# Kernel optimization log

Measured on AMD Instinct MI355X. Metric: run time of the kernel, lower is better.

Reference implementation:

```python
import jax, jax.numpy as jnp
import numpy as np

EPSILON = 0.1
MAX_ITER = 50

def setup_inputs() -> dict:
    key = jax.random.key(0)
    kx, ky = jax.random.split(key)
    x = jax.random.normal(kx, (16, 1024, 256), dtype=jnp.float32)
    y = jax.random.normal(ky, (16, 1024, 256), dtype=jnp.float32)
    return {"x": x, "y": y}

def _cdist(x, y):
    # pairwise euclidean distance, (B, Lx, Ly)
    x2 = jnp.sum(x * x, axis=-1)  # (B, Lx)
    y2 = jnp.sum(y * y, axis=-1)  # (B, Ly)
    xy = jnp.einsum('bld,bmd->blm', x, y)
    d2 = x2[:, :, None] + y2[:, None, :] - 2.0 * xy
    return jnp.sqrt(jnp.maximum(d2, 0.0))

def reference(x, y):
    cost = _cdist(x, y)                      # (B, Lx, Ly)
    B, Lx, Ly = cost.shape
    log_mu = jnp.full((B, Lx), -jnp.log(jnp.float32(Lx)), dtype=cost.dtype)
    log_nu = jnp.full((B, Ly), -jnp.log(jnp.float32(Ly)), dtype=cost.dtype)
    log_k = -cost / EPSILON                  # (B, Lx, Ly)

    def body(carry, _):
        log_u, log_v = carry
        log_u = log_mu - jax.scipy.special.logsumexp(log_k + log_v[:, None, :], axis=2)
        log_v = log_nu - jax.scipy.special.logsumexp(log_k + log_u[:, :, None], axis=1)
        return (log_u, log_v), None

    init = (jnp.zeros((B, Lx), cost.dtype), jnp.zeros((B, Ly), cost.dtype))
    (log_u, log_v), _ = jax.lax.scan(body, init, None, length=MAX_ITER)

    # transport = u * exp(log_k) * v, fused in log space
    transport = jnp.exp(log_u[:, :, None] + log_k + log_v[:, None, :])
    distance = jnp.sum(transport * cost, axis=(1, 2))  # (B,)
    return jnp.mean(distance)
```

## Files before the change

### kernel.cpp

```cpp
#include <hip/hip_runtime.h>
#include <math.h>

#define NB 16
#define L 1024
#define D 256
#define N_ITER 50
#define LOG_MU (-6.9314718055994531f)
#define QSCALE 2560.0f
#define QS (1.0f/256.0f)
#define QSC (1.0f/2560.0f)

typedef short short4_t __attribute__((ext_vector_type(4)));

__global__ __launch_bounds__(256) void norms_kernel(
    const float* __restrict__ x, const float* __restrict__ y,
    float* __restrict__ x2, float* __restrict__ y2) {
  int wid = threadIdx.x >> 6, lane = threadIdx.x & 63;
  int row = blockIdx.x * 4 + wid;
  const float* src = (row < NB * L) ? (x + (size_t)row * D)
                                    : (y + (size_t)(row - NB * L) * D);
  float4 v = *(const float4*)(src + lane * 4);
  float s = v.x * v.x + v.y * v.y + v.z * v.z + v.w * v.w;
  #pragma unroll
  for (int off = 32; off; off >>= 1) s += __shfl_down(s, off);
  if (lane == 0) {
    if (row < NB * L) x2[row] = s;
    else              y2[row - NB * L] = s;
  }
}

__global__ __launch_bounds__(256) void anchor_kernel(
    const float* __restrict__ x, const float* __restrict__ y,
    const float* __restrict__ x2, const float* __restrict__ y2,
    float* __restrict__ anchor) {
  int w = threadIdx.x >> 6, lane = threadIdx.x & 63;
  int gr = blockIdx.x * 4 + w;
  int b = gr >> 10, i = gr & 1023;
  const float* xr = x + (size_t)gr * D;
  float4 xv = *(const float4*)(xr + lane * 4);
  float dots[16];
  #pragma unroll
  for (int s = 0; s < 16; ++s) {
    int j = (i + s * 64 + s * s) & 1023;
    float4 yv = *(const float4*)(y + ((size_t)b * L + j) * D + lane * 4);
    dots[s] = xv.x * yv.x + xv.y * yv.y + xv.z * yv.z + xv.w * yv.w;
  }
  #pragma unroll
  for (int s = 0; s < 16; ++s)
    #pragma unroll
    for (int off = 32; off; off >>= 1) dots[s] += __shfl_xor(dots[s], off);
  if (lane == 0) {
    float xx = x2[gr];
    float mn = 3.4e38f;
    #pragma unroll
    for (int s = 0; s < 16; ++s) {
      int j = (i + s * 64 + s * s) & 1023;
      float d2 = xx + y2[b * L + j] - 2.0f * dots[s];
      mn = fminf(mn, sqrtf(fmaxf(d2, 0.0f)));
    }
    anchor[gr] = mn;
  }
}

__global__ __launch_bounds__(256) void costq_kernel(
    const float* __restrict__ x, const float* __restrict__ y,
    const float* __restrict__ x2, const float* __restrict__ y2,
    const float* __restrict__ anchor, short* __restrict__ Q) {
  __shared__ float xs[16][68];
  __shared__ float ys[16][68];
  int bid = blockIdx.x;
  int b = bid >> 8;
  int rem = bid & 255;
  int i0 = (rem >> 4) << 6;
  int j0 = (rem & 15) << 6;
  int tid = threadIdx.x;
  int tx = tid & 15, ty = tid >> 4;
  int r = tid >> 2, kq = tid & 3;

  float acc[4][4] = {};
  const float* xbase = x + ((size_t)b * L + i0 + r) * D + kq * 4;
  const float* ybase = y + ((size_t)b * L + j0 + r) * D + kq * 4;
  for (int k0 = 0; k0 < D; k0 += 16) {
    float4 xv = *(const float4*)(xbase + k0);
    float4 yv = *(const float4*)(ybase + k0);
    __syncthreads();
    xs[kq * 4 + 0][r] = xv.x; xs[kq * 4 + 1][r] = xv.y;
    xs[kq * 4 + 2][r] = xv.z; xs[kq * 4 + 3][r] = xv.w;
    ys[kq * 4 + 0][r] = yv.x; ys[kq * 4 + 1][r] = yv.y;
    ys[kq * 4 + 2][r] = yv.z; ys[kq * 4 + 3][r] = yv.w;
    __syncthreads();
    #pragma unroll
    for (int kk = 0; kk < 16; ++kk) {
      float4 av = *(const float4*)&xs[kk][ty * 4];
      float4 bv = *(const float4*)&ys[kk][tx * 4];
      float a[4] = {av.x, av.y, av.z, av.w};
      float bb[4] = {bv.x, bv.y, bv.z, bv.w};
      #pragma unroll
      for (int er = 0; er < 4; ++er)
        #pragma unroll
        for (int ec = 0; ec < 4; ++ec)
          acc[er][ec] = fmaf(a[er], bb[ec], acc[er][ec]);
    }
  }
  float xr[4], yc[4], ar[4];
  #pragma unroll
  for (int e = 0; e < 4; ++e) {
    xr[e] = x2[b * L + i0 + ty * 4 + e];
    yc[e] = y2[b * L + j0 + tx * 4 + e];
    ar[e] = anchor[b * L + i0 + ty * 4 + e];
  }
  #pragma unroll
  for (int er = 0; er < 4; ++er) {
    short4_t q4;
    #pragma unroll
    for (int ec = 0; ec < 4; ++ec) {
      float d2 = xr[er] + yc[ec] - 2.0f * acc[er][ec];
      float c = sqrtf(fmaxf(d2, 0.0f));
      int qi = __float2int_rn((ar[er] - c) * QSCALE);
      q4[ec] = (short)min(max(qi, -32767), 32767);
    }
    *(short4_t*)(Q + ((size_t)b * L + i0 + ty * 4 + er) * L + j0 + tx * 4) = q4;
  }
}

__global__ __launch_bounds__(256) void pass_fused_kernel(
    const short* __restrict__ Q, const float* __restrict__ anchor,
    const float* __restrict__ vin, float* __restrict__ uout,
    float* __restrict__ partial) {
  __shared__ float4 cacc[4][256];
  int bb = blockIdx.x;
  int w = threadIdx.x >> 6, lane = threadIdx.x & 63;
  int b = bb >> 6;
  const float4* g4 = (const float4*)(vin + (b << 10));
  float vv[16];
  float4 a0 = g4[lane * 2], a1 = g4[lane * 2 + 1];
  float4 a2 = g4[128 + lane * 2], a3 = g4[128 + lane * 2 + 1];
  vv[0]=a0.x; vv[1]=a0.y; vv[2]=a0.z; vv[3]=a0.w;
  vv[4]=a1.x; vv[5]=a1.y; vv[6]=a1.z; vv[7]=a1.w;
  vv[8]=a2.x; vv[9]=a2.y; vv[10]=a2.z; vv[11]=a2.w;
  vv[12]=a3.x; vv[13]=a3.y; vv[14]=a3.z; vv[15]=a3.w;
  float m = vv[0];
  #pragma unroll
  for (int t = 1; t < 16; ++t) m = fmaxf(m, vv[t]);
  #pragma unroll
  for (int off = 32; off; off >>= 1) m = fmaxf(m, __shfl_xor(m, off));
  #pragma unroll
  for (int t = 0; t < 16; ++t) vv[t] -= m;
  float E = __expf(LOG_MU - m);
  float colacc[16] = {};

  #define T8(base, V4)                                                   \
    t[base+0] = __expf(fmaf((float)(short)(V4.x), QS, vv[base+0]));      \
    t[base+1] = __expf(fmaf((float)((V4.x) >> 16), QS, vv[base+1]));     \
    t[base+2] = __expf(fmaf((float)(short)(V4.y), QS, vv[base+2]));      \
    t[base+3] = __expf(fmaf((float)((V4.y) >> 16), QS, vv[base+3]));     \
    t[base+4] = __expf(fmaf((float)(short)(V4.z), QS, vv[base+4]));      \
    t[base+5] = __expf(fmaf((float)(V4.z) >> 16), QS, vv[base+5]));      \
    t[base+6] = __expf(fmaf((float)(short)(V4.w), QS, vv[base+6]));      \
    t[base+7] = __expf(fmaf((float)((V4.w) >> 16), QS, vv[base+7]));

  #pragma unroll
  for (int rr = 0; rr < 4; ++rr) {
    int r = bb * 16 + rr * 4 + w;
    const int4* q0 = (const int4*)(Q + (size_t)r * L);
    int4 cA = q0[lane], cB = q0[64 + lane];
    float t[16];
    t[0]  = __expf(fmaf((float)(short)(cA.x), QS, vv[0]));
    t[1]  = __expf(fmaf((float)(cA.x >> 16),  QS, vv[1]));
    t[2]  = __expf(fmaf((float)(short)(cA.y), QS, vv[2]));
    t[3]  = __expf(fmaf((float)(cA.y >> 16),  QS, vv[3]));
    t[4]  = __expf(fmaf((float)(short)(cA.z), QS, vv[4]));
    t[5]  = __expf(fmaf((float)(cA.z >> 16),  QS, vv[5]));
    t[6]  = __expf(fmaf((float)(short)(cA.w), QS, vv[6]));
    t[7]  = __expf(fmaf((float)(cA.w >> 16),  QS, vv[7]));
    t[8]  = __expf(fmaf((float)(short)(cB.x), QS, vv[8]));
    t[9]  = __expf(fmaf((float)(cB.x >> 16),  QS, vv[9]));
    t[10] = __expf(fmaf((float)(short)(cB.y), QS, vv[10]));
    t[11] = __expf(fmaf((float)(cB.y >> 16),  QS, vv[11]));
    t[12] = __expf(fmaf((float)(short)(cB.z), QS, vv[12]));
    t[13] = __expf(fmaf((float)(cB.z >> 16),  QS, vv[13]));
    t[14] = __expf(fmaf((float)(short)(cB.w), QS, vv[14]));
    t[15] = __expf(fmaf((float)(cB.w >> 16),  QS, vv[15]));
    float racc = 0.0f;
    #pragma unroll
    for (int k = 0; k < 16; ++k) racc += t[k];
    #pragma unroll
    for (int off = 32; off; off >>= 1) racc += __shfl_xor(racc, off);
    if (lane == 0)
      uout[r] = LOG_MU + fmaf(10.0f, anchor[r], -m) - __logf(racc);
    float g = E / racc;
    #pragma unroll
    for (int k = 0; k < 16; ++k) colacc[k] = fmaf(t[k], g, colacc[k]);
  }
  cacc[w][lane * 2]       = {colacc[0], colacc[1], colacc[2], colacc[3]};
  cacc[w][lane * 2 + 1]   = {colacc[4], colacc[5], colacc[6], colacc[7]};
  cacc[w][128 + lane * 2]     = {colacc[8], colacc[9], colacc[10], colacc[11]};
  cacc[w][128 + lane * 2 + 1] = {colacc[12], colacc[13], colacc[14], colacc[15]};
  __syncthreads();
  int tid = threadIdx.x;
  float4 s0 = cacc[0][tid], s1 = cacc[1][tid], s2 = cacc[2][tid], s3 = cacc[3][tid];
  float4 s = {s0.x + s1.x + s2.x + s3.x, s0.y + s1.y + s2.y + s3.y,
              s0.z + s1.z + s2.z + s3.z, s0.w + s1.w + s2.w + s3.w};
  ((float4*)partial)[bb * 256 + tid] = s;
}

__global__ __launch_bounds__(256) void reducev_kernel(
    const float* __restrict__ partial, const float* __restrict__ vin,
    float* __restrict__ vout) {
  __shared__ float red[4];
  int b = blockIdx.x >> 2;
  int tid = threadIdx.x;
  const float* vb = vin + (b << 10);
  float m = fmaxf(fmaxf(vb[tid], vb[tid + 256]), fmaxf(vb[tid + 512], vb[tid + 768]));
  #pragma unroll
  for (int off = 32; off; off >>= 1) m = fmaxf(m, __shfl_xor(m, off));
  int w = tid >> 6;
  if ((tid & 63) == 0) red[w] = m;
  __syncthreads();
  m = fmaxf(fmaxf(red[0], red[1]), fmaxf(red[2], red[3]));
  int j = ((blockIdx.x & 3) << 8) + tid;
  const float* p = partial + (((size_t)b << 6) << 10) + j;
  float s = 0.0f;
  #pragma unroll
  for (int k = 0; k < 64; ++k) s += p[k << 10];
  vout[(b << 10) + j] = LOG_MU - __logf(s) + vb[j] - m;
}

__global__ __launch_bounds__(256) void distance_kernel(
    const short* __restrict__ Q, const float* __restrict__ anchor,
    const float* __restrict__ lu, const float* __restrict__ lv,
    float* __restrict__ pdist) {
  __shared__ float red[4];
  int bb = blockIdx.x;
  int w = threadIdx.x >> 6, lane = threadIdx.x & 63;
  int b = bb >> 6;
  const float4* g4 = (const float4*)(lv + (b << 10));
  float vv[16];
  float4 a0 = g4[lane * 2], a1 = g4[lane * 2 + 1];
  float4 a2 = g4[128 + lane * 2], a3 = g4[128 + lane * 2 + 1];
  vv[0]=a0.x; vv[1]=a0.y; vv[2]=a0.z; vv[3]=a0.w;
  vv[4]=a1.x; vv[5]=a1.y; vv[6]=a1.z; vv[7]=a1.w;
  vv[8]=a2.x; vv[9]=a2.y; vv[10]=a2.z; vv[11]=a2.w;
  vv[12]=a3.x; vv[13]=a3.y; vv[14]=a3.z; vv[15]=a3.w;
  float m = vv[0];
  #pragma unroll
  for (int t = 1; t < 16; ++t) m = fmaxf(m, vv[t]);
  #pragma unroll
  for (int off = 32; off; off >>= 1) m = fmaxf(m, __shfl_xor(m, off));
  #pragma unroll
  for (int t = 0; t < 16; ++t) vv[t] -= m;

  float racc = 0.0f;
  #pragma unroll
  for (int rr = 0; rr < 4; ++rr) {
    int r = bb * 16 + rr * 4 + w;
    float ar = anchor[r];
    float A = fmaf(-10.0f, ar, lu[r]) + m;
    float va[16];
    #pragma unroll
    for (int k = 0; k < 16; ++k) va[k] = vv[k] + A;
    const int4* q0 = (const int4*)(Q + (size_t)r * L);
    int4 cA = q0[lane], cB = q0[64 + lane];
    #define DACC(V, B)                                                      \
      { float qf = (float)(short)(V);                                       \
        float e = __expf(fmaf(qf, QS, va[B]));                              \
        racc = fmaf(e, fmaf(qf, -QSC, ar), racc);                           \
        qf = (float)((V) >> 16);                                            \
        e = __expf(fmaf(qf, QS, va[(B) + 1]));                              \
        racc = fmaf(e, fmaf(qf, -QSC, ar), racc); }
    DACC(cA.x, 0) DACC(cA.y, 2) DACC(cA.z, 4) DACC(cA.w, 6)
    DACC(cB.x, 8) DACC(cB.y, 10) DACC(cB.z, 12) DACC(cB.w, 14)
    #undef DACC
  }
  #pragma unroll
  for (int off = 32; off; off >>= 1) racc += __shfl_xor(racc, off);
  if (lane == 0) red[w] = racc;
  __syncthreads();
  if (threadIdx.x == 0) pdist[bb] = red[0] + red[1] + red[2] + red[3];
}

__global__ __launch_bounds__(256) void finalred_kernel(
    const float* __restrict__ pdist, float* __restrict__ out) {
  __shared__ float red[4];
  int tid = threadIdx.x;
  float s = pdist[tid] + pdist[tid + 256] + pdist[tid + 512] + pdist[tid + 768];
  #pragma unroll
  for (int off = 32; off; off >>= 1) s += __shfl_xor(s, off);
  int w = tid >> 6;
  if ((tid & 63) == 0) red[w] = s;
  __syncthreads();
  if (tid == 0) out[0] = (red[0] + red[1] + red[2] + red[3]) * (1.0f / NB);
}

extern "C" void kernel_launch(void* const* d_in, const int* in_sizes, int n_in,
                              void* d_out, int out_size, void* d_ws, size_t ws_size,
                              hipStream_t stream) {
  const float* x = (const float*)d_in[0];
  const float* y = (const float*)d_in[1];
  float* out = (float*)d_out;
  char* ws = (char*)d_ws;

  const size_t szQ = (size_t)NB * L * L * sizeof(short);
  const size_t szP = (size_t)NB * 64 * L * sizeof(float);
  short* Q = (short*)ws;
  float* partial = (float*)(ws + szQ);
  float* x2 = (float*)(ws + szQ + szP);
  float* y2 = x2 + NB * L;
  float* anchor = y2 + NB * L;
  float* lu = anchor + NB * L;
  float* lv = lu + NB * L;
  float* pdist = lv + NB * L;

  hipMemsetAsync(lv, 0, NB * L * sizeof(float), stream);

  norms_kernel<<<2 * NB * L / 4, 256, 0, stream>>>(x, y, x2, y2);
  anchor_kernel<<<NB * L / 4, 256, 0, stream>>>(x, y, x2, y2, anchor);
  costq_kernel<<<NB * 256, 256, 0, stream>>>(x, y, x2, y2, anchor, Q);

  for (int t = 0; t < N_ITER; ++t) {
    pass_fused_kernel<<<NB * L / 16, 256, 0, stream>>>(Q, anchor, lv, lu, partial);
    reducev_kernel<<<NB * L / 256, 256, 0, stream>>>(partial, lv, lv);
  }
  distance_kernel<<<NB * L / 16, 256, 0, stream>>>(Q, anchor, lu, lv, pdist);
  finalred_kernel<<<1, 256, 0, stream>>>(pdist, out);
}
```

Before: 835.0 us.

## Switch to base-2 log domain, fp16 cost storage, precomputed block maxima

Stores the quantized cost as fp16 instead of int16 and runs the Sinkhorn potentials in base-2 log space, so exp2f replaces __expf with the scale folded into constants. The per-batch max of v is now produced by reducev as 16 block maxima instead of a full 1024-wide max reduction in every pass block. reducev is split into more blocks with shared-memory partial sums, Q row loads are all issued up front, and costq gets register prefetch of the next k-slice. The fp16 encoding changes quantization precision relative to the int16 scheme.

```diff
diff --git a/kernel.cpp b/kernel.cpp
--- a/kernel.cpp
+++ b/kernel.cpp
@@ -1,14 +1,17 @@
 #include <hip/hip_runtime.h>
+#include <hip/hip_fp16.h>
 #include <math.h>
 
 #define NB 16
 #define L 1024
 #define D 256
 #define N_ITER 50
-#define LOG_MU (-6.9314718055994531f)
 #define QSCALE 2560.0f
-#define QS (1.0f/256.0f)
 #define QSC (1.0f/2560.0f)
+#define LOG2E 1.4426950408889634f
+#define QS2 (LOG2E/256.0f)
+#define LOG_MU2 (-10.0f)
+#define TEN_LOG2E 14.426950408889634f
 
 typedef short short4_t __attribute__((ext_vector_type(4)));
 
@@ -32,7 +35,7 @@
 __global__ __launch_bounds__(256) void anchor_kernel(
     const float* __restrict__ x, const float* __restrict__ y,
     const float* __restrict__ x2, const float* __restrict__ y2,
-    float* __restrict__ anchor) {
+    float* __restrict__ anchor, float* __restrict__ A2) {
   int w = threadIdx.x >> 6, lane = threadIdx.x & 63;
   int gr = blockIdx.x * 4 + w;
   int b = gr >> 10, i = gr & 1023;
@@ -59,13 +62,14 @@
       mn = fminf(mn, sqrtf(fmaxf(d2, 0.0f)));
     }
     anchor[gr] = mn;
+    A2[gr] = mn * TEN_LOG2E;
   }
 }
 
 __global__ __launch_bounds__(256) void costq_kernel(
     const float* __restrict__ x, const float* __restrict__ y,
     const float* __restrict__ x2, const float* __restrict__ y2,
-    const float* __restrict__ anchor, short* __restrict__ Q) {
+    const float* __restrict__ anchor, __half* __restrict__ Q) {
   __shared__ float xs[16][68];
   __shared__ float ys[16][68];
   int bid = blockIdx.x;
@@ -80,9 +84,12 @@
   float acc[4][4] = {};
   const float* xbase = x + ((size_t)b * L + i0 + r) * D + kq * 4;
   const float* ybase = y + ((size_t)b * L + j0 + r) * D + kq * 4;
+  float4 xv = *(const float4*)(xbase);
+  float4 yv = *(const float4*)(ybase);
   for (int k0 = 0; k0 < D; k0 += 16) {
-    float4 xv = *(const float4*)(xbase + k0);
-    float4 yv = *(const float4*)(ybase + k0);
+    int kn = (k0 + 16) & 255;
+    float4 nx = *(const float4*)(xbase + kn);
+    float4 ny = *(const float4*)(ybase + kn);
     __syncthreads();
     xs[kq * 4 + 0][r] = xv.x; xs[kq * 4 + 1][r] = xv.y;
     xs[kq * 4 + 2][r] = xv.z; xs[kq * 4 + 3][r] = xv.w;
@@ -101,6 +108,7 @@
         for (int ec = 0; ec < 4; ++ec)
           acc[er][ec] = fmaf(a[er], bb[ec], acc[er][ec]);
     }
+    xv = nx; yv = ny;
   }
   float xr[4], yc[4], ar[4];
   #pragma unroll
@@ -116,167 +124,201 @@
     for (int ec = 0; ec < 4; ++ec) {
       float d2 = xr[er] + yc[ec] - 2.0f * acc[er][ec];
       float c = sqrtf(fmaxf(d2, 0.0f));
-      int qi = __float2int_rn((ar[er] - c) * QSCALE);
-      q4[ec] = (short)min(max(qi, -32767), 32767);
+      float qv = fminf(fmaxf((ar[er] - c) * QSCALE, -30000.0f), 30000.0f);
+      __half h = __float2half(qv);
+      q4[ec] = __half_as_short(h);
     }
-    *(short4_t*)(Q + ((size_t)b * L + i0 + ty * 4 + er) * L + j0 + tx * 4) = q4;
-  }
-}
+    *(short4_t*)((short*)Q + ((size_t)b * L + i0 + ty * 4 + er) * L + j0 + tx * 4) = q4;
+  }
+}
+
+#define DEC2(word, base)                                           \
+  { __half2 h2 = *reinterpret_cast<const __half2*>(&(word));       \
+    float2 f2 = __half22float2(h2);                                \
+    t[base]     = exp2f(fmaf(f2.x, QS2, vv[base]));                \
+    t[base + 1] = exp2f(fmaf(f2.y, QS2, vv[base + 1])); }
 
 __global__ __launch_bounds__(256) void pass_fused_kernel(
-    const short* __restrict__ Q, const float* __restrict__ anchor,
-    const float* __restrict__ vin, float* __restrict__ uout,
-    float* __restrict__ partial) {
+    const __half* __restrict__ Q, const float* __restrict__ A2,
+    const float* __restrict__ v2, const float* __restrict__ bmax,
+    float* __restrict__ u2out, float* __restrict__ partial) {
   __shared__ float4 cacc[4][256];
   int bb = blockIdx.x;
-  int w = threadIdx.x >> 6, lane = threadIdx.x & 63;
+  int tid = threadIdx.x;
+  int w = tid >> 6, lane = tid & 63;
   int b = bb >> 6;
-  const float4* g4 = (const float4*)(vin + (b << 10));
-  float vv[16];
+  int r0 = bb * 16 + w;
+
+  const int4* q0 = (const int4*)(Q + (size_t)r0 * L);
+  const int4* q1 = (const int4*)(Q + (size_t)(r0 + 4) * L);
+  const int4* q2 = (const int4*)(Q + (size_t)(r0 + 8) * L);
+  const int4* q3 = (const int4*)(Q + (size_t)(r0 + 12) * L);
+  int4 cA0 = q0[lane], cB0 = q0[64 + lane];
+  int4 cA1 = q1[lane], cB1 = q1[64 + lane];
+  int4 cA2 = q2[lane], cB2 = q2[64 + lane];
+  int4 cA3 = q3[lane], cB3 = q3[64 + lane];
+
+  const float* bm = bmax + b * 16;
+  float m2 = bm[0];
+  #pragma unroll
+  for (int k = 1; k < 16; ++k) m2 = fmaxf(m2, bm[k]);
+
+  const float4* g4 = (const float4*)(v2 + (b << 10));
   float4 a0 = g4[lane * 2], a1 = g4[lane * 2 + 1];
   float4 a2 = g4[128 + lane * 2], a3 = g4[128 + lane * 2 + 1];
+  float vv[16];
+  vv[0]=a0.x-m2; vv[1]=a0.y-m2; vv[2]=a0.z-m2; vv[3]=a0.w-m2;
+  vv[4]=a1.x-m2; vv[5]=a1.y-m2; vv[6]=a1.z-m2; vv[7]=a1.w-m2;
+  vv[8]=a2.x-m2; vv[9]=a2.y-m2; vv[10]=a2.z-m2; vv[11]=a2.w-m2;
+  vv[12]=a3.x-m2; vv[13]=a3.y-m2; vv[14]=a3.z-m2; vv[15]=a3.w-m2;
+  float E2 = exp2f(LOG_MU2 - m2);
+  float colacc[16] = {};
+  float r_0, r_1, r_2, r_3;
+
+#define ROWP(cA_, cB_, ROUT)                                              \
+  { float t[16];                                                          \
+    DEC2(cA_.x, 0) DEC2(cA_.y, 2) DEC2(cA_.z, 4) DEC2(cA_.w, 6)           \
+    DEC2(cB_.x, 8) DEC2(cB_.y, 10) DEC2(cB_.z, 12) DEC2(cB_.w, 14)        \
+    float racc = ((t[0]+t[1])+(t[2]+t[3])) + ((t[4]+t[5])+(t[6]+t[7]))    \
+               + ((t[8]+t[9])+(t[10]+t[11])) + ((t[12]+t[13])+(t[14]+t[15])); \
+    _Pragma("unroll")                                                     \
+    for (int off = 32; off; off >>= 1) racc += __shfl_xor(racc, off);     \
+    float g = E2 / racc;                                                  \
+    _Pragma("unroll")                                                     \
+    for (int k = 0; k < 16; ++k) colacc[k] = fmaf(t[k], g, colacc[k]);    \
+    ROUT = racc; }
+
+  ROWP(cA0, cB0, r_0)
+  ROWP(cA1, cB1, r_1)
+  ROWP(cA2, cB2, r_2)
+  ROWP(cA3, cB3, r_3)
+#undef ROWP
+
+  if (lane == 0) {
+    u2out[r0]      = LOG_MU2 + A2[r0]      - m2 - log2f(r_0);
+    u2out[r0 + 4]  = LOG_MU2 + A2[r0 + 4]  - m2 - log2f(r_1);
+    u2out[r0 + 8]  = LOG_MU2 + A2[r0 + 8]  - m2 - log2f(r_2);
+    u2out[r0 + 12] = LOG_MU2 + A2[r0 + 12] - m2 - log2f(r_3);
+  }
+  cacc[w][lane * 2]           = {colacc[0], colacc[1], colacc[2], colacc[3]};
+  cacc[w][lane * 2 + 1]       = {colacc[4], colacc[5], colacc[6], colacc[7]};
+  cacc[w][128 + lane * 2]     = {colacc[8], colacc[9], colacc[10], colacc[11]};
+  cacc[w][128 + lane * 2 + 1] = {colacc[12], colacc[13], colacc[14], colacc[15]};
+  __syncthreads();
+  float4 s0 = cacc[0][tid], s1 = cacc[1][tid], s2 = cacc[2][tid], s3 = cacc[3][tid];
+  float4 s = {s0.x + s1.x + s2.x + s3.x, s0.y + s1.y + s2.y + s3.y,
+              s0.z + s1.z + s2.z + s3.z, s0.w + s1.w + s2.w + s3.w};
+  ((float4*)partial)[bb * 256 + tid] = s;
+}
+
+__global__ __launch_bounds__(256) void reducev_kernel(
+    const float* __restrict__ partial, float* __restrict__ v2,
+    const float* __restrict__ bmax_cur, float* __restrict__ bmax_next) {
+  __shared__ float ss[4][64];
+  int blk = blockIdx.x;
+  int b = blk >> 4;
+  int j0 = (blk & 15) << 6;
+  int tid = threadIdx.x;
+  int c = tid & 63, q = tid >> 6;
+  const float* p = partial + (((size_t)b * 64 + q * 16) << 10) + j0 + c;
+  float s = 0.0f;
+  #pragma unroll
+  for (int k = 0; k < 16; ++k) s += p[(size_t)k << 10];
+  ss[q][c] = s;
+  __syncthreads();
+  if (tid < 64) {
+    const float* bm = bmax_cur + b * 16;
+    float m2 = bm[0];
+    #pragma unroll
+    for (int k = 1; k < 16; ++k) m2 = fmaxf(m2, bm[k]);
+    float S = ss[0][c] + ss[1][c] + ss[2][c] + ss[3][c];
+    int j = (b << 10) + j0 + c;
+    float vn = LOG_MU2 - log2f(S) + v2[j] - m2;
+    v2[j] = vn;
+    float mx = vn;
+    #pragma unroll
+    for (int off = 32; off; off >>= 1) mx = fmaxf(mx, __shfl_xor(mx, off));
+    if (c == 0) bmax_next[blk] = mx;
+  }
+}
+
+__global__ __launch_bounds__(256) void distance_kernel(
+    const __half* __restrict__ Q, const float* __restrict__ anchor,
+    const float* __restrict__ A2, const float* __restrict__ u2,
+    const float* __restrict__ v2, float* __restrict__ pdist) {
+  __shared__ float red[4];
+  int bb = blockIdx.x;
+  int tid = threadIdx.x;
+  int w = tid >> 6, lane = tid & 63;
+  int b = bb >> 6;
+  int r0 = bb * 16 + w;
+  const int4* q0 = (const int4*)(Q + (size_t)r0 * L);
+  const int4* q1 = (const int4*)(Q + (size_t)(r0 + 4) * L);
+  const int4* q2 = (const int4*)(Q + (size_t)(r0 + 8) * L);
+  const int4* q3 = (const int4*)(Q + (size_t)(r0 + 12) * L);
+  int4 cA0 = q0[lane], cB0 = q0[64 + lane];
+  int4 cA1 = q1[lane], cB1 = q1[64 + lane];
+  int4 cA2 = q2[lane], cB2 = q2[64 + lane];
+  int4 cA3 = q3[lane], cB3 = q3[64 + lane];
+
+  const float4* g4 = (const float4*)(v2 + (b << 10));
+  float4 a0 = g4[lane * 2], a1 = g4[lane * 2 + 1];
+  float4 a2 = g4[128 + lane * 2], a3 = g4[128 + lane * 2 + 1];
+  float vv[16];
   vv[0]=a0.x; vv[1]=a0.y; vv[2]=a0.z; vv[3]=a0.w;
   vv[4]=a1.x; vv[5]=a1.y; vv[6]=a1.z; vv[7]=a1.w;
   vv[8]=a2.x; vv[9]=a2.y; vv[10]=a2.z; vv[11]=a2.w;
   vv[12]=a3.x; vv[13]=a3.y; vv[14]=a3.z; vv[15]=a3.w;
-  float m = vv[0];
-  #pragma unroll
-  for (int t = 1; t < 16; ++t) m = fmaxf(m, vv[t]);
-  #pragma unroll
-  for (int off = 32; off; off >>= 1) m = fmaxf(m, __shfl_xor(m, off));
-  #pragma unroll
-  for (int t = 0; t < 16; ++t) vv[t] -= m;
-  float E = __expf(LOG_MU - m);
-  float colacc[16] = {};
-
-  #define T8(base, V4)                                                   \
-    t[base+0] = __expf(fmaf((float)(short)(V4.x), QS, vv[base+0]));      \
-    t[base+1] = __expf(fmaf((float)((V4.x) >> 16), QS, vv[base+1]));     \
-    t[base+2] = __expf(fmaf((float)(short)(V4.y), QS, vv[base+2]));      \
-    t[base+3] = __expf(fmaf((float)((V4.y) >> 16), QS, vv[base+3]));     \
-    t[base+4] = __expf(fmaf((float)(short)(V4.z), QS, vv[base+4]));      \
-    t[base+5] = __expf(fmaf((float)(V4.z) >> 16), QS, vv[base+5]));      \
-    t[base+6] = __expf(fmaf((float)(short)(V4.w), QS, vv[base+6]));      \
-    t[base+7] = __expf(fmaf((float)((V4.w) >> 16), QS, vv[base+7]));
-
-  #pragma unroll
-  for (int rr = 0; rr < 4; ++rr) {
-    int r = bb * 16 + rr * 4 + w;
-    const int4* q0 = (const int4*)(Q + (size_t)r * L);
-    int4 cA = q0[lane], cB = q0[64 + lane];
-    float t[16];
-    t[0]  = __expf(fmaf((float)(short)(cA.x), QS, vv[0]));
-    t[1]  = __expf(fmaf((float)(cA.x >> 16),  QS, vv[1]));
-    t[2]  = __expf(fmaf((float)(short)(cA.y), QS, vv[2]));
-    t[3]  = __expf(fmaf((float)(cA.y >> 16),  QS, vv[3]));
-    t[4]  = __expf(fmaf((float)(short)(cA.z), QS, vv[4]));
-    t[5]  = __expf(fmaf((float)(cA.z >> 16),  QS, vv[5]));
-    t[6]  = __expf(fmaf((float)(short)(cA.w), QS, vv[6]));
-    t[7]  = __expf(fmaf((float)(cA.w >> 16),  QS, vv[7]));
-    t[8]  = __expf(fmaf((float)(short)(cB.x), QS, vv[8]));
-    t[9]  = __expf(fmaf((float)(cB.x >> 16),  QS, vv[9]));
-    t[10] = __expf(fmaf((float)(short)(cB.y), QS, vv[10]));
-    t[11] = __expf(fmaf((float)(cB.y >> 16),  QS, vv[11]));
-    t[12] = __expf(fmaf((float)(short)(cB.z), QS, vv[12]));
-    t[13] = __expf(fmaf((float)(cB.z >> 16),  QS, vv[13]));
-    t[14] = __expf(fmaf((float)(short)(cB.w), QS, vv[14]));
-    t[15] = __expf(fmaf((float)(cB.w >> 16),  QS, vv[15]));
-    float racc = 0.0f;
-    #pragma unroll
-    for (int k = 0; k < 16; ++k) racc += t[k];
-    #pragma unroll
-    for (int off = 32; off; off >>= 1) racc += __shfl_xor(racc, off);
-    if (lane == 0)
-      uout[r] = LOG_MU + fmaf(10.0f, anchor[r], -m) - __logf(racc);
-    float g = E / racc;
-    #pragma unroll
-    for (int k = 0; k < 16; ++k) colacc[k] = fmaf(t[k], g, colacc[k]);
-  }
-  cacc[w][lane * 2]       = {colacc[0], colacc[1], colacc[2], colacc[3]};
-  cacc[w][lane * 2 + 1]   = {colacc[4], colacc[5], colacc[6], colacc[7]};
-  cacc[w][128 + lane * 2]     = {colacc[8], colacc[9], colacc[10], colacc[11]};
-  cacc[w][128 + lane * 2 + 1] = {colacc[12], colacc[13], colacc[14], colacc[15]};
-  __syncthreads();
-  int tid = threadIdx.x;
-  float4 s0 = cacc[0][tid], s1 = cacc[1][tid], s2 = cacc[2][tid], s3 = cacc[3][tid];
-  float4 s = {s0.x + s1.x + s2.x + s3.x, s0.y + s1.y + s2.y + s3.y,
-              s0.z + s1.z + s2.z + s3.z, s0.w + s1.w + s2.w + s3.w};
-  ((float4*)partial)[bb * 256 + tid] = s;
-}
-
-__global__ __launch_bounds__(256) void reducev_kernel(
-    const float* __restrict__ partial, const float* __restrict__ vin,
-    float* __restrict__ vout) {
-  __shared__ float red[4];
-  int b = blockIdx.x >> 2;
-  int tid = threadIdx.x;
-  const float* vb = vin + (b << 10);
-  float m = fmaxf(fmaxf(vb[tid], vb[tid + 256]), fmaxf(vb[tid + 512], vb[tid + 768]));
-  #pragma unroll
-  for (int off = 32; off; off >>= 1) m = fmaxf(m, __shfl_xor(m, off));
-  int w = tid >> 6;
-  if ((tid & 63) == 0) red[w] = m;
-  __syncthreads();
-  m = fmaxf(fmaxf(red[0], red[1]), fmaxf(red[2], red[3]));
-  int j = ((blockIdx.x & 3) << 8) + tid;
-  const float* p = partial + (((size_t)b << 6) << 10) + j;
-  float s = 0.0f;
-  #pragma unroll
-  for (int k = 0; k < 64; ++k) s += p[k << 10];
-  vout[(b << 10) + j] = LOG_MU - __logf(s) + vb[j] - m;
-}
-
-__global__ __launch_bounds__(256) void distance_kernel(
-    const short* __restrict__ Q, const float* __restrict__ anchor,
-    const float* __restrict__ lu, const float* __restrict__ lv,
-    float* __restrict__ pdist) {
-  __shared__ float red[4];
-  int bb = blockIdx.x;
-  int w = threadIdx.x >> 6, lane = threadIdx.x & 63;
-  int b = bb >> 6;
-  const float4* g4 = (const float4*)(lv + (b << 10));
-  float vv[16];
-  float4 a0 = g4[lane * 2], a1 = g4[lane * 2 + 1];
-  float4 a2 = g4[128 + lane * 2], a3 = g4[128 + lane * 2 + 1];
-  vv[0]=a0.x; vv[1]=a0.y; vv[2]=a0.z; vv[3]=a0.w;
-  vv[4]=a1.x; vv[5]=a1.y; vv[6]=a1.z; vv[7]=a1.w;
-  vv[8]=a2.x; vv[9]=a2.y; vv[10]=a2.z; vv[11]=a2.w;
-  vv[12]=a3.x; vv[13]=a3.y; vv[14]=a3.z; vv[15]=a3.w;
-  float m = vv[0];
-  #pragma unroll
-  for (int t = 1; t < 16; ++t) m = fmaxf(m, vv[t]);
-  #pragma unroll
-  for (int off = 32; off; off >>= 1) m = fmaxf(m, __shfl_xor(m, off));
-  #pragma unroll
-  for (int t = 0; t < 16; ++t) vv[t] -= m;
 
   float racc = 0.0f;
-  #pragma unroll
-  for (int rr = 0; rr < 4; ++rr) {
-    int r = bb * 16 + rr * 4 + w;
-    float ar = anchor[r];
-    float A = fmaf(-10.0f, ar, lu[r]) + m;
-    float va[16];
-    #pragma unroll
-    for (int k = 0; k < 16; ++k) va[k] = vv[k] + A;
-    const int4* q0 = (const int4*)(Q + (size_t)r * L);
-    int4 cA = q0[lane], cB = q0[64 + lane];
-    #define DACC(V, B)                                                      \
-      { float qf = (float)(short)(V);                                       \
-        float e = __expf(fmaf(qf, QS, va[B]));                              \
-        racc = fmaf(e, fmaf(qf, -QSC, ar), racc);                           \
-        qf = (float)((V) >> 16);                                            \
-        e = __expf(fmaf(qf, QS, va[(B) + 1]));                              \
-        racc = fmaf(e, fmaf(qf, -QSC, ar), racc); }
-    DACC(cA.x, 0) DACC(cA.y, 2) DACC(cA.z, 4) DACC(cA.w, 6)
-    DACC(cB.x, 8) DACC(cB.y, 10) DACC(cB.z, 12) DACC(cB.w, 14)
-    #undef DACC
-  }
+#define DROW(cA_, cB_, ROFF)                                              \
+  { int r = r0 + ROFF;                                                    \
+    float ar = anchor[r];                                                 \
+    float base = u2[r] - A2[r];                                           \
+    float va[16];                                                         \
+    _Pragma("unroll")                                                     \
+    for (int k = 0; k < 16; ++k) va[k] = vv[k] + base;                    \
+    float t[16];                                                          \
+    { float* vvsave = va; float* vv = vvsave;                             \
+      DEC2(cA_.x, 0) DEC2(cA_.y, 2) DEC2(cA_.z, 4) DEC2(cA_.w, 6)         \
+      DEC2(cB_.x, 8) DEC2(cB_.y, 10) DEC2(cB_.z, 12) DEC2(cB_.w, 14) }    \
+    __half2 h2; float2 f2;                                                \
+    h2 = *reinterpret_cast<const __half2*>(&cA_.x); f2 = __half22float2(h2); \
+    racc = fmaf(t[0], fmaf(f2.x, -QSC, ar), racc);                        \
+    racc = fmaf(t[1], fmaf(f2.y, -QSC, ar), racc);                        \
+    h2 = *reinterpret_cast<const __half2*>(&cA_.y); f2 = __half22float2(h2); \
+    racc = fmaf(t[2], fmaf(f2.x, -QSC, ar), racc);                        \
+    racc = fmaf(t[3], fmaf(f2.y, -QSC, ar), racc);                        \
+    h2 = *reinterpret_cast<const __half2*>(&cA_.z); f2 = __half22float2(h2); \
+    racc = fmaf(t[4], fmaf(f2.x, -QSC, ar), racc);                        \
+    racc = fmaf(t[5], fmaf(f2.y, -QSC, ar), racc);                        \
+    h2 = *reinterpret_cast<const __half2*>(&cA_.w); f2 = __half22float2(h2); \
+    racc = fmaf(t[6], fmaf(f2.x, -QSC, ar), racc);                        \
+    racc = fmaf(t[7], fmaf(f2.y, -QSC, ar), racc);                        \
+    h2 = *reinterpret_cast<const __half2*>(&cB_.x); f2 = __half22float2(h2); \
+    racc = fmaf(t[8], fmaf(f2.x, -QSC, ar), racc);                        \
+    racc = fmaf(t[9], fmaf(f2.y, -QSC, ar), racc);                        \
+    h2 = *reinterpret_cast<const __half2*>(&cB_.y); f2 = __half22float2(h2); \
+    racc = fmaf(t[10], fmaf(f2.x, -QSC, ar), racc);                       \
+    racc = fmaf(t[11], fmaf(f2.y, -QSC, ar), racc);                       \
+    h2 = *reinterpret_cast<const __half2*>(&cB_.z); f2 = __half22float2(h2); \
+    racc = fmaf(t[12], fmaf(f2.x, -QSC, ar), racc);                       \
+    racc = fmaf(t[13], fmaf(f2.y, -QSC, ar), racc);                       \
+    h2 = *reinterpret_cast<const __half2*>(&cB_.w); f2 = __half22float2(h2); \
+    racc = fmaf(t[14], fmaf(f2.x, -QSC, ar), racc);                       \
+    racc = fmaf(t[15], fmaf(f2.y, -QSC, ar), racc); }
+
+  DROW(cA0, cB0, 0)
+  DROW(cA1, cB1, 4)
+  DROW(cA2, cB2, 8)
+  DROW(cA3, cB3, 12)
+#undef DROW
+
   #pragma unroll
   for (int off = 32; off; off >>= 1) racc += __shfl_xor(racc, off);
   if (lane == 0) red[w] = racc;
   __syncthreads();
-  if (threadIdx.x == 0) pdist[bb] = red[0] + red[1] + red[2] + red[3];
+  if (tid == 0) pdist[bb] = red[0] + red[1] + red[2] + red[3];
 }
 
 __global__ __launch_bounds__(256) void finalred_kernel(
@@ -300,27 +342,34 @@
   float* out = (float*)d_out;
   char* ws = (char*)d_ws;
 
-  const size_t szQ = (size_t)NB * L * L * sizeof(short);
+  const size_t szQ = (size_t)NB * L * L * sizeof(__half);
   const size_t szP = (size_t)NB * 64 * L * sizeof(float);
-  short* Q = (short*)ws;
+  __half* Q = (__half*)ws;
   float* partial = (float*)(ws + szQ);
   float* x2 = (float*)(ws + szQ + szP);
   float* y2 = x2 + NB * L;
   float* anchor = y2 + NB * L;
-  float* lu = anchor + NB * L;
+  float* A2 = anchor + NB * L;
+  float* lu = A2 + NB * L;
   float* lv = lu + NB * L;
-  float* pdist = lv + NB * L;
+  float* bmA = lv + NB * L;
+  float* bmB = bmA + 256;
+  float* pdist = bmB + 256;
 
   hipMemsetAsync(lv, 0, NB * L * sizeof(float), stream);
+  hipMemsetAsync(bmA, 0, 256 * sizeof(float), stream);
 
   norms_kernel<<<2 * NB * L / 4, 256, 0, stream>>>(x, y, x2, y2);
-  anchor_kernel<<<NB * L / 4, 256, 0, stream>>>(x, y, x2, y2, anchor);
+  anchor_kernel<<<NB * L / 4, 256, 0, stream>>>(x, y, x2, y2, anchor, A2);
   costq_kernel<<<NB * 256, 256, 0, stream>>>(x, y, x2, y2, anchor, Q);
 
+  float* bmc = bmA;
+  float* bmn = bmB;
   for (int t = 0; t < N_ITER; ++t) {
-    pass_fused_kernel<<<NB * L / 16, 256, 0, stream>>>(Q, anchor, lv, lu, partial);
-    reducev_kernel<<<NB * L / 256, 256, 0, stream>>>(partial, lv, lv);
-  }
-  distance_kernel<<<NB * L / 16, 256, 0, stream>>>(Q, anchor, lu, lv, pdist);
+    pass_fused_kernel<<<NB * 64, 256, 0, stream>>>(Q, A2, lv, bmc, lu, partial);
+    reducev_kernel<<<NB * 16, 256, 0, stream>>>(partial, lv, bmc, bmn);
+    float* tmp = bmc; bmc = bmn; bmn = tmp;
+  }
+  distance_kernel<<<NB * 64, 256, 0, stream>>>(Q, anchor, A2, lu, lv, pdist);
   finalred_kernel<<<1, 256, 0, stream>>>(pdist, out);
 }
```

New measurement: 881.1 us. 1.06x slower.
